# Performance work log

Hardware: AMD Instinct MI355X
Metric: run time of the kernel (lower is better)

## Reference

```python
import jax, jax.numpy as jnp
import numpy as np

GDEP = 2
ALPHA = 0.05


def _mixprop(x, adj, W, b):
    # x: [B, C, N, T], adj: [N, N] (row v aggregates neighbors w)
    N = adj.shape[0]
    adj = adj + jnp.eye(N, dtype=adj.dtype)
    a = adj / jnp.sum(adj, axis=1, keepdims=True)  # row-normalized
    h = x
    outs = [h]
    for _ in range(GDEP):
        # nconv: einsum('ncwl,vw->ncvl')
        h = ALPHA * x + (1.0 - ALPHA) * jnp.einsum('bcwl,vw->bcvl', h, a)
        outs.append(h)
    ho = jnp.concatenate(outs, axis=1)  # [B, (GDEP+1)*C, N, T]
    # 1x1 Conv2d == channel-mixing matmul
    return jnp.einsum('bcnl,oc->bonl', ho, W) + b[None, :, None, None]


def setup_inputs() -> dict:
    key = jax.random.key(0)
    ks = jax.random.split(key, 6)
    B, C, N, T = 8, 32, 512, 168
    C_cat, C_out = (GDEP + 1) * C, 32
    return {
        'x': jax.random.normal(ks[0], (B, C, N, T), dtype=jnp.float32),
        'adp': jax.random.uniform(ks[1], (N, N), dtype=jnp.float32),
        'W1': jax.random.normal(ks[2], (C_out, C_cat), dtype=jnp.float32) * 0.1,
        'b1': jax.random.normal(ks[3], (C_out,), dtype=jnp.float32) * 0.1,
        'W2': jax.random.normal(ks[4], (C_out, C_cat), dtype=jnp.float32) * 0.1,
        'b2': jax.random.normal(ks[5], (C_out,), dtype=jnp.float32) * 0.1,
    }


def reference(x, adp, W1, b1, W2, b2):
    return _mixprop(x, adp, W1, b1) + _mixprop(x, adp.T, W2, b2)
```

## Files before the change

kernel.cpp:

```cpp
#include <hip/hip_runtime.h>
#include <stdint.h>

#define BDIM 8
#define CDIM 32
#define NDIM 512
#define TDIM 168
#define KG   2048
#define NJ   43008
#define ALPHA_ 0.05f
#define BETA_  0.95f

typedef __attribute__((ext_vector_type(8))) short short8;
typedef __attribute__((ext_vector_type(4))) float f32x4;
typedef __attribute__((ext_vector_type(2))) float f2v;
typedef __attribute__((ext_vector_type(4))) unsigned short u16x4;

__device__ __forceinline__ unsigned short f2bf(float f) {
  union { float f; unsigned int u; } v; v.f = f;
  unsigned int r = v.u + 0x7fffu + ((v.u >> 16) & 1u);
  return (unsigned short)(r >> 16);
}
__device__ __forceinline__ float bf2f(unsigned short h) {
  union { unsigned int u; float f; } v; v.u = ((unsigned int)h) << 16;
  return v.f;
}
__device__ __forceinline__ unsigned char f2fp8(float f) {
  union { float f; unsigned u; } v; v.f = f;
  unsigned s = (v.u >> 24) & 0x80u;
  unsigned au = v.u & 0x7fffffffu;
  if (au >= 0x43e80000u) return (unsigned char)(s | 0x7eu);
  if (au < 0x3c800000u) {
    float a = (f < 0.f) ? -f : f;
    unsigned m = (unsigned)(a * 512.f + 0.5f);
    return (unsigned char)(s | (m > 7 ? 8u : m));
  }
  unsigned e8 = au >> 23;
  unsigned m23 = au & 0x7fffffu;
  unsigned rm = m23 + 0x7ffffu + ((m23 >> 20) & 1u);
  if (rm >= 0x800000u) { rm -= 0x800000u; e8 += 1u; }
  unsigned e4 = e8 - 120u;
  return (unsigned char)(s | (e4 << 3) | (rm >> 20));
}
__device__ __forceinline__ unsigned int pack4fp8(float a, float b, float c, float d) {
#if __has_builtin(__builtin_amdgcn_cvt_pk_fp8_f32)
  int r = __builtin_amdgcn_cvt_pk_fp8_f32(a, b, 0, false);
  r = __builtin_amdgcn_cvt_pk_fp8_f32(c, d, r, true);
  return (unsigned int)r;
#else
  return (unsigned)f2fp8(a) | ((unsigned)f2fp8(b) << 8) |
         ((unsigned)f2fp8(c) << 16) | ((unsigned)f2fp8(d) << 24);
#endif
}
__device__ __forceinline__ void gload_lds16(const void* g, void* l) {
  __builtin_amdgcn_global_load_lds((const __attribute__((address_space(1))) void*)g,
                                   (__attribute__((address_space(3))) void*)l, 16, 0, 0);
}

__global__ void gc_prep2(const float* __restrict__ adp,
                         const float* __restrict__ W1, const float* __restrict__ b1,
                         const float* __restrict__ W2, const float* __restrict__ b2,
                         float* __restrict__ Af, unsigned char* __restrict__ G2f,
                         unsigned short* __restrict__ Ub, float* __restrict__ bias) {
  int t = threadIdx.x;
  if (blockIdx.x == 512) {
    for (int idx = t; idx < 160 * 32; idx += 256) {
      int ko = idx >> 5, c = idx & 31, o = ko & 31, s = ko >> 5;
      float v;
      if (s == 0)      v = BETA_ * (W1[o * 96 + 32 + c] + ALPHA_ * W1[o * 96 + 64 + c]);
      else if (s == 1) v = BETA_ * BETA_ * W1[o * 96 + 64 + c];
      else if (s == 2) v = BETA_ * (W2[o * 96 + 32 + c] + ALPHA_ * W2[o * 96 + 64 + c]);
      else if (s == 3) v = BETA_ * BETA_ * W2[o * 96 + 64 + c];
      else             v = W1[o * 96 + c] + ALPHA_ * (W1[o * 96 + 32 + c] + W1[o * 96 + 64 + c])
                         + W2[o * 96 + c] + ALPHA_ * (W2[o * 96 + 32 + c] + W2[o * 96 + 64 + c]);
      Ub[idx] = f2bf(v);
    }
    if (t < 32) bias[t] = b1[t] + b2[t];
    return;
  }
  int v = blockIdx.x;
  float sA = 0.f, sB = 0.f;
  for (int w = t; w < NDIM; w += 256) { sA += adp[v * NDIM + w]; sB += adp[w * NDIM + v]; }
  __shared__ float red[2][256];
  red[0][t] = sA; red[1][t] = sB; __syncthreads();
  for (int s = 128; s > 0; s >>= 1) {
    if (t < s) { red[0][t] += red[0][t + s]; red[1][t] += red[1][t + s]; }
    __syncthreads();
  }
  float ra = 1.f / (1.f + red[0][0]);
  float rb = 1.f / (1.f + red[1][0]);
  for (int w = t; w < NDIM; w += 256) {
    float d = (v == w) ? 1.f : 0.f;
    float a  = (adp[v * NDIM + w] + d) * ra;
    float a2 = (adp[w * NDIM + v] + d) * rb;
    Af[(size_t)v * NDIM + w] = a;
    Af[(size_t)NDIM * NDIM + (size_t)v * NDIM + w] = a2;
    G2f[((size_t)((0  + (w >> 4)) * 512) + v) * 16 + (w & 15)] = f2fp8(a * 64.f);
    G2f[((size_t)((64 + (w >> 4)) * 512) + v) * 16 + (w & 15)] = f2fp8(a2 * 64.f);
  }
}

__global__ __launch_bounds__(256, 4) void gc_sq2(const float* __restrict__ Af,
                                                 unsigned char* __restrict__ G2f) {
  int bid = blockIdx.x;
  int mat = bid >> 8, tile = bid & 255;
  int v0 = (tile >> 4) * 32, w0 = (tile & 15) * 32;
  const float* M = Af + (size_t)mat * NDIM * NDIM;
  __shared__ float T1[64][33];
  __shared__ float T2[64][33];
  int t = threadIdx.x;
  int ty = t >> 4, tx = t & 15;
  float a00 = 0.f, a01 = 0.f, a10 = 0.f, a11 = 0.f;
  for (int u0 = 0; u0 < NDIM; u0 += 64) {
    #pragma unroll
    for (int q = 0; q < 8; ++q) {
      int id = q * 256 + t;
      int c = id & 63, r = id >> 6;
      T1[c][r] = M[(size_t)(v0 + r) * NDIM + u0 + c];
      int u = id >> 5, w = id & 31;
      T2[u][w] = M[(size_t)(u0 + u) * NDIM + w0 + w];
    }
    __syncthreads();
    for (int u = 0; u < 64; ++u) {
      f2v a = *(const f2v*)&T1[u][ty * 2];
      f2v b = *(const f2v*)&T2[u][tx * 2];
      a00 += a[0] * b[0]; a01 += a[0] * b[1];
      a10 += a[1] * b[0]; a11 += a[1] * b[1];
    }
    __syncthreads();
  }
  int base = mat ? 96 : 32;
  int v = v0 + ty * 2, w = w0 + tx * 2;
  size_t cb  = (size_t)((base + (w >> 4)) * 512) * 16;
  size_t cb1 = (size_t)((base + ((w + 1) >> 4)) * 512) * 16;
  G2f[cb  + (size_t)(v    ) * 16 + (w & 15)]       = f2fp8(a00 * 64.f);
  G2f[cb1 + (size_t)(v    ) * 16 + ((w + 1) & 15)] = f2fp8(a01 * 64.f);
  G2f[cb  + (size_t)(v + 1) * 16 + (w & 15)]       = f2fp8(a10 * 64.f);
  G2f[cb1 + (size_t)(v + 1) * 16 + ((w + 1) & 15)] = f2fp8(a11 * 64.f);
}

__global__ __launch_bounds__(256, 2) void gc_mix6(const float* __restrict__ x,
    const unsigned short* __restrict__ Ub, unsigned char* __restrict__ Pgf,
    unsigned short* __restrict__ R0) {
  __shared__ __align__(16) unsigned short xs[26880];
  int bid = blockIdx.x;
  int lq = bid & 3, wt = (bid >> 2) & 31, b = bid >> 7;
  int l0 = lq * 42, w0 = wt * 16;
  int tid = threadIdx.x, wv = tid >> 6, lane = tid & 63;
  int l15 = lane & 15, hi = lane >> 4;

  #pragma unroll 4
  for (int e = 0; e < 84; ++e) {
    int id = e * 256 + tid;
    int c = id / 672, rem = id - c * 672;
    int w = rem / 42, ll = rem - w * 42;
    float v = x[(size_t)((b * 32 + c) * 512 + w0 + w) * 168 + l0 + ll];
    xs[(ll * 16 + (w ^ (ll & 15))) * 40 + c] = f2bf(v);
  }
  __syncthreads();

  short8 uF[10];
  #pragma unroll
  for (int mt = 0; mt < 10; ++mt)
    uF[mt] = *(const short8*)(Ub + (size_t)(mt * 16 + l15) * 32 + hi * 8);

  for (int i = 0; i < 11; ++i) {
    int li = wv + 4 * i;
    if (li >= 42) break;
    int l = l0 + li;
    short8 xf = *(const short8*)&xs[(li * 16 + (l15 ^ (li & 15))) * 40 + hi * 8];
    size_t jbase = (size_t)(b * 168 + l) * 32;
    #pragma unroll
    for (int mt = 0; mt < 10; ++mt) {
      f32x4 z = {0.f, 0.f, 0.f, 0.f};
      f32x4 p = __builtin_amdgcn_mfma_f32_16x16x32_bf16(xf, uF[mt], z, 0, 0, 0);
      size_t jj = jbase + ((mt & 1) << 4) + l15;
      if (mt < 8) {
        int slice = mt >> 1;
        unsigned int pk = pack4fp8(p[0], p[1], p[2], p[3]);
        *(unsigned int*)(Pgf + ((size_t)(slice * 32 + wt) * NJ + jj) * 16 + hi * 4) = pk;
      } else {
        int r0c = wt * 2 + (hi >> 1);
        u16x4 pk16 = { f2bf(p[0]), f2bf(p[1]), f2bf(p[2]), f2bf(p[3]) };
        *(u16x4*)(R0 + ((size_t)r0c * NJ + jj) * 8 + (hi & 1) * 4) = pk16;
      }
    }
  }
}

__global__ __launch_bounds__(256, 2) void gc_gemm9c(const unsigned char* __restrict__ G2f,
    const unsigned char* __restrict__ Pgf, const unsigned short* __restrict__ R0,
    const float* __restrict__ bias, float* __restrict__ out) {
  int bid = blockIdx.x;
  int swz = (bid & 7) * 84 + (bid >> 3);
  int mt = swz & 1, jt = swz >> 1;
  int n0 = mt * 256, jj0 = jt * 128;

  __shared__ __align__(16) unsigned char SH[36864];
  unsigned char* AbBase = SH;
  unsigned char* BbBase = SH + 24576;

  int tid = threadIdx.x, lane = tid & 63, wid = tid >> 6;
  int wm = wid >> 1, wn = wid & 1;
  int l15 = lane & 15, hi = lane >> 4;

  const unsigned char* srcA[2]; int dA[2];
  #pragma unroll
  for (int q = 0; q < 2; ++q) {
    int f = q * 256 + tid;
    srcA[q] = G2f + ((size_t)(f >> 8) * 512 + n0 + (f & 255)) * 16;
    dA[q] = f * 16;
  }
  int g = tid;
  const unsigned char* srcB0 = Pgf + ((size_t)(g >> 7) * NJ + jj0 + (g & 127)) * 16;
  int dB0 = g * 16;
  const size_t strideA = 2 * 512 * 16;
  const size_t strideB = (size_t)2 * NJ * 16;

  f32x4 acc[8][4] = {};

  #pragma unroll
  for (int q = 0; q < 2; ++q) gload_lds16(srcA[q], AbBase + dA[q]);
  gload_lds16(srcB0, BbBase + dB0);
  #pragma unroll
  for (int q = 0; q < 2; ++q) gload_lds16(srcA[q] + strideA, AbBase + 8192 + dA[q]);
  gload_lds16(srcB0 + strideB, BbBase + 4096 + dB0);

  int aoffs = (hi >> 1) * 4096 + (wm * 128 + l15) * 16 + (hi & 1) * 8;
  int boffs = (hi >> 1) * 2048 + (wn * 64 + l15) * 16 + (hi & 1) * 8;

  int cur = 0;
  for (int t = 0; t < 64; ++t) {
    if (t < 63) { asm volatile("s_waitcnt vmcnt(3)" ::: "memory"); }
    else        { asm volatile("s_waitcnt vmcnt(0)" ::: "memory"); }
    __builtin_amdgcn_s_barrier();

    if (t < 62) {
      int nxt = cur - 1; if (nxt < 0) nxt = 2;
      #pragma unroll
      for (int q = 0; q < 2; ++q)
        gload_lds16(srcA[q] + (size_t)(t + 2) * strideA, AbBase + nxt * 8192 + dA[q]);
      gload_lds16(srcB0 + (size_t)(t + 2) * strideB, BbBase + nxt * 4096 + dB0);
    }

    const unsigned char* ap = AbBase + cur * 8192;
    const unsigned char* bp = BbBase + cur * 4096;
    long aF[8]; long bF[4];
    #pragma unroll
    for (int mi = 0; mi < 8; ++mi)
      aF[mi] = *(const long*)(ap + aoffs + mi * 256);
    #pragma unroll
    for (int nj = 0; nj < 4; ++nj)
      bF[nj] = *(const long*)(bp + boffs + nj * 256);

    #pragma unroll
    for (int mi = 0; mi < 8; ++mi)
      #pragma unroll
      for (int nj = 0; nj < 4; ++nj)
        acc[mi][nj] = __builtin_amdgcn_mfma_f32_16x16x32_fp8_fp8(aF[mi], bF[nj], acc[mi][nj], 0, 0, 0);

    cur = cur + 1; if (cur == 3) cur = 0;
  }

  int bl0 = jt * 4;
  int bq = bl0 / 168, l0g = bl0 - bq * 168;
  float* Cs = (float*)SH;
  int o = tid & 31, nl8 = tid >> 5;
  float bs = bias[o];
  __syncthreads();
  for (int s = 0; s < 4; ++s) {
    if (wm == (s >> 1)) {
      int mio = (s & 1) * 4;
      #pragma unroll
      for (int mi = 0; mi < 4; ++mi)
        #pragma unroll
        for (int nj = 0; nj < 4; ++nj) {
          int row = mi * 16 + hi * 4;
          int col = wn * 64 + nj * 16 + l15;
          #pragma unroll
          for (int r = 0; r < 4; ++r)
            Cs[(row + r) * 132 + col] = acc[mio + mi][nj][r] * 0.015625f;
        }
    }
    __syncthreads();
    int n_g0 = n0 + s * 64 + nl8 * 8;
    const unsigned short* p4c =
        R0 + ((size_t)(n_g0 >> 3) * NJ + (size_t)bl0 * 32 + o) * 8;
    short8 pv0 = *(const short8*)(p4c);
    short8 pv1 = *(const short8*)(p4c + 256);
    short8 pv2 = *(const short8*)(p4c + 512);
    short8 pv3 = *(const short8*)(p4c + 768);
    #pragma unroll
    for (int q = 0; q < 8; ++q) {
      int nr = nl8 * 8 + q;
      int n_g = n_g0 + q;
      float v0 = Cs[nr * 132 +  0 + o] + bf2f((unsigned short)pv0[q]) + bs;
      float v1 = Cs[nr * 132 + 32 + o] + bf2f((unsigned short)pv1[q]) + bs;
      float v2 = Cs[nr * 132 + 64 + o] + bf2f((unsigned short)pv2[q]) + bs;
      float v3 = Cs[nr * 132 + 96 + o] + bf2f((unsigned short)pv3[q]) + bs;
      f32x4 vv = {v0, v1, v2, v3};
      *(f32x4*)(out + ((size_t)(bq * 32 + o) * 512 + n_g) * 168 + l0g) = vv;
    }
    __syncthreads();
  }
}

extern "C" void kernel_launch(void* const* d_in, const int* in_sizes, int n_in,
                              void* d_out, int out_size, void* d_ws, size_t ws_size,
                              hipStream_t stream) {
  const float* x   = (const float*)d_in[0];
  const float* adp = (const float*)d_in[1];
  const float* W1  = (const float*)d_in[2];
  const float* b1  = (const float*)d_in[3];
  const float* W2  = (const float*)d_in[4];
  const float* b2  = (const float*)d_in[5];
  float* out = (float*)d_out;

  char* w = (char*)d_ws;
  unsigned char*  Pgf = (unsigned char*)(w);
  unsigned short* R0  = (unsigned short*)(w + 88080384ULL);
  unsigned char*  G2f = (unsigned char*)(w + 132120576ULL);
  float* Af           = (float*)(w + 133169152ULL);
  unsigned short* Ub  = (unsigned short*)(w + 135266304ULL);
  float* bias         = (float*)(w + 135282688ULL);
  if (ws_size < 135282816ULL) return;

  gc_prep2<<<513, 256, 0, stream>>>(adp, W1, b1, W2, b2, Af, G2f, Ub, bias);
  gc_sq2<<<512, 256, 0, stream>>>(Af, G2f);
  gc_mix6<<<1024, 256, 0, stream>>>(x, Ub, Pgf, R0);
  gc_gemm9c<<<672, 256, 0, stream>>>(G2f, Pgf, R0, bias, out);
}
```

Measured before the change: 197.4 us.

## Switch fp8 GEMM to 32x32x64 scaled MFMA with doubled K-step tiles

Replaces the 16x16x32 fp8 MFMA inner loop with the gfx950 32x32x64 f8f6f4 scaled MFMA (unit scales). K per stage is doubled, so the pipeline runs 32 iterations instead of 64, and the triple-buffered LDS grows to 72KB. Operand fragments become 32-byte loads and the accumulator layout changes, so the epilogue's row mapping is rewritten. The goal is higher MFMA throughput and fewer barriers per tile. The cost is more LDS per block, which may limit the 2-blocks-per-CU occupancy target.

```diff
diff --git a/kernel.cpp b/kernel.cpp
--- a/kernel.cpp
+++ b/kernel.cpp
@@ -12,8 +12,11 @@
 
 typedef __attribute__((ext_vector_type(8))) short short8;
 typedef __attribute__((ext_vector_type(4))) float f32x4;
+typedef __attribute__((ext_vector_type(16))) float f32x16;
 typedef __attribute__((ext_vector_type(2))) float f2v;
 typedef __attribute__((ext_vector_type(4))) unsigned short u16x4;
+typedef __attribute__((ext_vector_type(4))) int i32x4;
+typedef __attribute__((ext_vector_type(8))) int i32x8;
 
 __device__ __forceinline__ unsigned short f2bf(float f) {
   union { float f; unsigned int u; } v; v.f = f;
@@ -187,7 +190,7 @@
   }
 }
 
-__global__ __launch_bounds__(256, 2) void gc_gemm9c(const unsigned char* __restrict__ G2f,
+__global__ __launch_bounds__(256, 2) void gc_gemm15(const unsigned char* __restrict__ G2f,
     const unsigned char* __restrict__ Pgf, const unsigned short* __restrict__ R0,
     const float* __restrict__ bias, float* __restrict__ out) {
   int bid = blockIdx.x;
@@ -195,68 +198,82 @@
   int mt = swz & 1, jt = swz >> 1;
   int n0 = mt * 256, jj0 = jt * 128;
 
-  __shared__ __align__(16) unsigned char SH[36864];
+  __shared__ __align__(16) unsigned char SH[73728];
   unsigned char* AbBase = SH;
-  unsigned char* BbBase = SH + 24576;
+  unsigned char* BbBase = SH + 49152;
 
   int tid = threadIdx.x, lane = tid & 63, wid = tid >> 6;
   int wm = wid >> 1, wn = wid & 1;
-  int l15 = lane & 15, hi = lane >> 4;
-
-  const unsigned char* srcA[2]; int dA[2];
+  int lo = lane & 31, hs = lane >> 5;
+
+  const unsigned char* srcA[4]; int dA[4];
+  #pragma unroll
+  for (int q = 0; q < 4; ++q) {
+    srcA[q] = G2f + ((size_t)(q * 512) + n0 + tid) * 16;
+    dA[q] = (q * 256 + tid) * 16;
+  }
+  const unsigned char* srcB[2]; int dB[2];
   #pragma unroll
   for (int q = 0; q < 2; ++q) {
-    int f = q * 256 + tid;
-    srcA[q] = G2f + ((size_t)(f >> 8) * 512 + n0 + (f & 255)) * 16;
-    dA[q] = f * 16;
-  }
-  int g = tid;
-  const unsigned char* srcB0 = Pgf + ((size_t)(g >> 7) * NJ + jj0 + (g & 127)) * 16;
-  int dB0 = g * 16;
-  const size_t strideA = 2 * 512 * 16;
-  const size_t strideB = (size_t)2 * NJ * 16;
-
-  f32x4 acc[8][4] = {};
-
-  #pragma unroll
-  for (int q = 0; q < 2; ++q) gload_lds16(srcA[q], AbBase + dA[q]);
-  gload_lds16(srcB0, BbBase + dB0);
-  #pragma unroll
-  for (int q = 0; q < 2; ++q) gload_lds16(srcA[q] + strideA, AbBase + 8192 + dA[q]);
-  gload_lds16(srcB0 + strideB, BbBase + 4096 + dB0);
-
-  int aoffs = (hi >> 1) * 4096 + (wm * 128 + l15) * 16 + (hi & 1) * 8;
-  int boffs = (hi >> 1) * 2048 + (wn * 64 + l15) * 16 + (hi & 1) * 8;
+    int g = q * 256 + tid;
+    srcB[q] = Pgf + ((size_t)(g >> 7) * NJ + jj0 + (g & 127)) * 16;
+    dB[q] = g * 16;
+  }
+  const size_t strideA = 4 * 512 * 16;
+  const size_t strideB = (size_t)4 * NJ * 16;
+
+  f32x16 acc[4][2] = {};
+
+  #pragma unroll
+  for (int q = 0; q < 4; ++q) gload_lds16(srcA[q], AbBase + dA[q]);
+  #pragma unroll
+  for (int q = 0; q < 2; ++q) gload_lds16(srcB[q], BbBase + dB[q]);
+  #pragma unroll
+  for (int q = 0; q < 4; ++q) gload_lds16(srcA[q] + strideA, AbBase + 16384 + dA[q]);
+  #pragma unroll
+  for (int q = 0; q < 2; ++q) gload_lds16(srcB[q] + strideB, BbBase + 8192 + dB[q]);
+
+  int aoffs = hs * 8192 + (wm * 128 + lo) * 16;
+  int boffs = hs * 4096 + (wn * 64 + lo) * 16;
 
   int cur = 0;
-  for (int t = 0; t < 64; ++t) {
-    if (t < 63) { asm volatile("s_waitcnt vmcnt(3)" ::: "memory"); }
+  for (int t = 0; t < 32; ++t) {
+    if (t < 31) { asm volatile("s_waitcnt vmcnt(6)" ::: "memory"); }
     else        { asm volatile("s_waitcnt vmcnt(0)" ::: "memory"); }
     __builtin_amdgcn_s_barrier();
 
-    if (t < 62) {
+    if (t < 30) {
       int nxt = cur - 1; if (nxt < 0) nxt = 2;
       #pragma unroll
+      for (int q = 0; q < 4; ++q)
+        gload_lds16(srcA[q] + (size_t)(t + 2) * strideA, AbBase + nxt * 16384 + dA[q]);
+      #pragma unroll
       for (int q = 0; q < 2; ++q)
-        gload_lds16(srcA[q] + (size_t)(t + 2) * strideA, AbBase + nxt * 8192 + dA[q]);
-      gload_lds16(srcB0 + (size_t)(t + 2) * strideB, BbBase + nxt * 4096 + dB0);
-    }
-
-    const unsigned char* ap = AbBase + cur * 8192;
-    const unsigned char* bp = BbBase + cur * 4096;
-    long aF[8]; long bF[4];
-    #pragma unroll
-    for (int mi = 0; mi < 8; ++mi)
-      aF[mi] = *(const long*)(ap + aoffs + mi * 256);
-    #pragma unroll
-    for (int nj = 0; nj < 4; ++nj)
-      bF[nj] = *(const long*)(bp + boffs + nj * 256);
-
-    #pragma unroll
-    for (int mi = 0; mi < 8; ++mi)
+        gload_lds16(srcB[q] + (size_t)(t + 2) * strideB, BbBase + nxt * 8192 + dB[q]);
+    }
+
+    const unsigned char* ap = AbBase + cur * 16384;
+    const unsigned char* bp = BbBase + cur * 8192;
+    i32x8 aF[4], bF[2];
+    #pragma unroll
+    for (int mi = 0; mi < 4; ++mi) {
+      i32x4 alo = *(const i32x4*)(ap + aoffs + mi * 512);
+      i32x4 ahi = *(const i32x4*)(ap + aoffs + mi * 512 + 4096);
+      aF[mi] = __builtin_shufflevector(alo, ahi, 0, 1, 2, 3, 4, 5, 6, 7);
+    }
+    #pragma unroll
+    for (int nj = 0; nj < 2; ++nj) {
+      i32x4 blo = *(const i32x4*)(bp + boffs + nj * 512);
+      i32x4 bhi = *(const i32x4*)(bp + boffs + nj * 512 + 2048);
+      bF[nj] = __builtin_shufflevector(blo, bhi, 0, 1, 2, 3, 4, 5, 6, 7);
+    }
+
+    #pragma unroll
+    for (int mi = 0; mi < 4; ++mi)
       #pragma unroll
-      for (int nj = 0; nj < 4; ++nj)
-        acc[mi][nj] = __builtin_amdgcn_mfma_f32_16x16x32_fp8_fp8(aF[mi], bF[nj], acc[mi][nj], 0, 0, 0);
+      for (int nj = 0; nj < 2; ++nj)
+        acc[mi][nj] = __builtin_amdgcn_mfma_scale_f32_32x32x64_f8f6f4(
+            aF[mi], bF[nj], acc[mi][nj], 0, 0, 0, 0x7F7F7F7F, 0, 0x7F7F7F7F);
 
     cur = cur + 1; if (cur == 3) cur = 0;
   }
@@ -269,16 +286,17 @@
   __syncthreads();
   for (int s = 0; s < 4; ++s) {
     if (wm == (s >> 1)) {
-      int mio = (s & 1) * 4;
+      int mib = (s & 1) * 2;
       #pragma unroll
-      for (int mi = 0; mi < 4; ++mi)
+      for (int mi2 = 0; mi2 < 2; ++mi2)
         #pragma unroll
-        for (int nj = 0; nj < 4; ++nj) {
-          int row = mi * 16 + hi * 4;
-          int col = wn * 64 + nj * 16 + l15;
+        for (int nj = 0; nj < 2; ++nj) {
+          int col = wn * 64 + nj * 32 + lo;
           #pragma unroll
-          for (int r = 0; r < 4; ++r)
-            Cs[(row + r) * 132 + col] = acc[mio + mi][nj][r] * 0.015625f;
+          for (int r = 0; r < 16; ++r) {
+            int row = mi2 * 32 + (r & 3) + 8 * (r >> 2) + 4 * hs;
+            Cs[row * 132 + col] = acc[mib + mi2][nj][r] * 0.015625f;
+          }
         }
     }
     __syncthreads();
@@ -327,5 +345,5 @@
   gc_prep2<<<513, 256, 0, stream>>>(adp, W1, b1, W2, b2, Af, G2f, Ub, bias);
   gc_sq2<<<512, 256, 0, stream>>>(Af, G2f);
   gc_mix6<<<1024, 256, 0, stream>>>(x, Ub, Pgf, R0);
-  gc_gemm9c<<<672, 256, 0, stream>>>(G2f, Pgf, R0, bias, out);
-}
+  gc_gemm15<<<672, 256, 0, stream>>>(G2f, Pgf, R0, bias, out);
+}
```

Result: faster. 172.7 us (-12.5%).
